# Kernel tuning notes

Hardware: AMD Instinct MI355X
Metric: run time of the kernel (lower is better)

Reference implementation:

```python
import jax, jax.numpy as jnp
import numpy as np

TOP_K = 2
CAPACITY_FACTOR = 1.0


def setup_inputs() -> dict:
    key = jax.random.key(0)
    ks = jax.random.split(key, 8)
    B, T, D, E = 4, 4096, 1024, 8
    H = 4 * D
    rn = lambda k, shape, sc: jax.random.normal(k, shape, jnp.float32) * sc
    return dict(
        x=rn(ks[0], (B, T, D), 1.0),
        noise_raw=rn(ks[1], (B, T, E), 1.0),  # replaces torch.randn_like
        Wr=rn(ks[2], (D, E), D ** -0.5), br=jnp.zeros((E,), jnp.float32),
        Wn=rn(ks[3], (D, E), D ** -0.5), bn=jnp.zeros((E,), jnp.float32),
        W1=rn(ks[4], (E, D, H), D ** -0.5), b1=jnp.zeros((E, H), jnp.float32),
        W2=rn(ks[5], (E, H, D), H ** -0.5), b2=jnp.zeros((E, D), jnp.float32),
    )


def reference(x, noise_raw, Wr, br, Wn, bn, W1, b1, W2, b2):
    B, T, D = x.shape
    E = Wr.shape[1]
    N = B * T

    # --- NoisyTopkRouter ---
    logits = x @ Wr + br                               # [B,T,E]
    noise_logits = x @ Wn + bn                         # [B,T,E]
    noisy = logits + noise_raw * jax.nn.softplus(noise_logits)
    top_vals, top_idx = jax.lax.top_k(noisy, TOP_K)    # [B,T,K]
    # softmax over (-inf)-masked sparse logits == softmax over the top-k values
    probs_k = jax.nn.softmax(top_vals, axis=-1)        # [B,T,K]
    onehot = jax.nn.one_hot(top_idx, E, dtype=x.dtype) # [B,T,K,E]
    router = jnp.einsum('btk,btke->bte', probs_k, onehot)  # sparse router probs

    # --- dispatch with capacity limit (first-come in flat token order) ---
    flat_x = x.reshape(N, D)
    flat_router = router.reshape(N, E)
    mask = onehot.reshape(N, TOP_K, E).sum(1) > 0      # [N,E] token n routed to expert e
    capacity = int(N * TOP_K / E * CAPACITY_FACTOR)
    # stable argsort brings selected tokens (key 0) first, preserving flat order
    order = jnp.argsort(jnp.where(mask, 0, 1), axis=0)             # [N,E]
    limited = order[:capacity].T                                   # [E,C] token ids (padded with unselected)
    keep = jnp.take_along_axis(mask, order[:capacity], axis=0).T   # [E,C] valid slots

    # --- grouped expert FFN ---
    xg = flat_x[limited]                                            # [E,C,D]
    h = jax.nn.relu(jnp.einsum('ecd,edh->ech', xg, W1) + b1[:, None, :])
    out_e = jnp.einsum('ech,ehd->ecd', h, W2) + b2[:, None, :]      # [E,C,D]
    # dropout is identity in eval mode

    # --- combine (scatter-add with gating; padded slots gated to 0) ---
    gate = flat_router[limited, jnp.arange(E)[:, None]] * keep.astype(x.dtype)  # [E,C]
    updates = jnp.zeros_like(flat_x).at[limited.reshape(-1)].add(
        (out_e * gate[..., None]).reshape(-1, D))
    return updates.reshape(B, T, D)
```

## Files before the change

### kernel.cpp

```cpp
#include <hip/hip_runtime.h>
#include <hip/hip_bf16.h>

namespace {
constexpr int kD = 1024, kE = 8, kH = 4096;
constexpr int kN = 16384;
constexpr int kCap = 4096;
}

typedef __attribute__((ext_vector_type(8))) short short8;
typedef __attribute__((ext_vector_type(4))) float f32x4;

static __device__ __forceinline__ unsigned short f2bf(float f) {
    __hip_bfloat16 h = __float2bfloat16(f);
    unsigned short s;
    __builtin_memcpy(&s, &h, 2);
    return s;
}

static __device__ __forceinline__ void gload_lds16(const unsigned short* g, unsigned short* l) {
    __builtin_amdgcn_global_load_lds(
        (const __attribute__((address_space(1))) unsigned int*)g,
        (__attribute__((address_space(3))) unsigned int*)l, 16, 0, 0);
}

__global__ __launch_bounds__(256) void moe_tcvt2(
    const float* __restrict__ W1, unsigned short* __restrict__ W1t,
    const float* __restrict__ W2, unsigned short* __restrict__ W2t)
{
    const int z = blockIdx.z;
    const float* src;
    unsigned short* dst;
    int R, C, bx, by;
    if (z < kE) {
        src = W1 + (size_t)z * kD * kH; dst = W1t + (size_t)z * kD * kH;
        R = kD; C = kH; bx = blockIdx.x % (kH / 64); by = blockIdx.x / (kH / 64);
    } else {
        src = W2 + (size_t)(z - kE) * kH * kD; dst = W2t + (size_t)(z - kE) * kH * kD;
        R = kH; C = kD; bx = blockIdx.x % (kD / 64); by = blockIdx.x / (kD / 64);
    }
    const int c0 = bx * 64, r0 = by * 64;
    __shared__ float t[64][68];
    const int tid = (int)threadIdx.x;
    const int tr = tid >> 2;
    const int tc = (tid & 3) * 16;
    #pragma unroll
    for (int j = 0; j < 4; ++j) {
        const float4 v = *(const float4*)(src + (size_t)(r0 + tr) * C + c0 + tc + j * 4);
        *(float4*)&t[tr][tc + j * 4] = v;
    }
    __syncthreads();
    unsigned short o[16];
    #pragma unroll
    for (int j = 0; j < 16; ++j) o[j] = f2bf(t[tc + j][tr]);
    unsigned short* dp = dst + (size_t)(c0 + tr) * R + r0 + tc;
    *(short8*)dp = *(const short8*)&o[0];
    *(short8*)(dp + 8) = *(const short8*)&o[8];
}

__global__ __launch_bounds__(256) void moe_router(
    const float* __restrict__ x, const float* __restrict__ noise_raw,
    const float* __restrict__ Wr, const float* __restrict__ br,
    const float* __restrict__ Wn, const float* __restrict__ bn,
    int2* __restrict__ topIdx, float2* __restrict__ topProb,
    unsigned short* __restrict__ xb, float* __restrict__ out)
{
    const int wave = threadIdx.x >> 6;
    const int lane = threadIdx.x & 63;
    const int n = blockIdx.x * 4 + wave;
    const float* xr = x + (size_t)n * kD;
    unsigned short* xbr = xb + (size_t)n * kD;
    float* outr = out + (size_t)n * kD;

    float accr[kE], accn[kE];
    #pragma unroll
    for (int e = 0; e < kE; ++e) { accr[e] = 0.f; accn[e] = 0.f; }

    const float4 z4 = make_float4(0.f, 0.f, 0.f, 0.f);
    #pragma unroll
    for (int c = 0; c < 4; ++c) {
        const int d0 = c * 256 + lane * 4;
        const float4 xv = *(const float4*)(xr + d0);
        *(float4*)(outr + d0) = z4;
        short4 bv;
        bv.x = (short)f2bf(xv.x); bv.y = (short)f2bf(xv.y);
        bv.z = (short)f2bf(xv.z); bv.w = (short)f2bf(xv.w);
        *(short4*)(xbr + d0) = bv;
        const float xs[4] = {xv.x, xv.y, xv.z, xv.w};
        #pragma unroll
        for (int j = 0; j < 4; ++j) {
            const float4* wr4 = (const float4*)(Wr + (size_t)(d0 + j) * kE);
            const float4* wn4 = (const float4*)(Wn + (size_t)(d0 + j) * kE);
            const float4 r0 = wr4[0], r1 = wr4[1];
            const float4 m0 = wn4[0], m1 = wn4[1];
            const float xj = xs[j];
            accr[0] += xj * r0.x; accr[1] += xj * r0.y; accr[2] += xj * r0.z; accr[3] += xj * r0.w;
            accr[4] += xj * r1.x; accr[5] += xj * r1.y; accr[6] += xj * r1.z; accr[7] += xj * r1.w;
            accn[0] += xj * m0.x; accn[1] += xj * m0.y; accn[2] += xj * m0.z; accn[3] += xj * m0.w;
            accn[4] += xj * m1.x; accn[5] += xj * m1.y; accn[6] += xj * m1.z; accn[7] += xj * m1.w;
        }
    }
    #pragma unroll
    for (int e = 0; e < kE; ++e) {
        #pragma unroll
        for (int off = 32; off >= 1; off >>= 1) {
            accr[e] += __shfl_xor(accr[e], off, 64);
            accn[e] += __shfl_xor(accn[e], off, 64);
        }
    }
    if (lane == 0) {
        float noisy[kE];
        #pragma unroll
        for (int e = 0; e < kE; ++e) {
            const float lg = accr[e] + br[e];
            const float nl = accn[e] + bn[e];
            const float sp = fmaxf(nl, 0.f) + log1pf(expf(-fabsf(nl)));
            noisy[e] = lg + noise_raw[(size_t)n * kE + e] * sp;
        }
        int i0 = 0;
        #pragma unroll
        for (int e = 1; e < kE; ++e) if (noisy[e] > noisy[i0]) i0 = e;
        int i1 = (i0 == 0) ? 1 : 0;
        #pragma unroll
        for (int e = 0; e < kE; ++e) if (e != i0 && noisy[e] > noisy[i1]) i1 = e;
        const float ex = expf(noisy[i1] - noisy[i0]);
        topIdx[n] = make_int2(i0, i1);
        topProb[n] = make_float2(1.f / (1.f + ex), ex / (1.f + ex));
    }
}

__global__ __launch_bounds__(256) void moe_dispatch(
    const int2* __restrict__ topIdx, const float2* __restrict__ topProb,
    int* __restrict__ tokList, float* __restrict__ gateList, int* __restrict__ cnt)
{
    const int e = blockIdx.x;
    const int lane = threadIdx.x & 63;
    const int wq = threadIdx.x >> 6;
    const int tpw = kN / 4;
    const unsigned long long below = (lane == 0) ? 0ull : ((~0ull) >> (64 - lane));
    __shared__ int cw[4];

    int mycnt = 0;
    for (int it = 0; it < tpw / 64; ++it) {
        const int n = wq * tpw + it * 64 + lane;
        const int2 ti = topIdx[n];
        const bool sel = (ti.x == e) || (ti.y == e);
        mycnt += __popcll(__ballot(sel));
    }
    if (lane == 0) cw[wq] = mycnt;
    __syncthreads();
    int base = 0;
    #pragma unroll
    for (int q = 0; q < 4; ++q) if (q < wq) base += cw[q];

    for (int it = 0; it < tpw / 64; ++it) {
        const int n = wq * tpw + it * 64 + lane;
        const int2 ti = topIdx[n];
        const float2 tp = topProb[n];
        const bool sel = (ti.x == e) || (ti.y == e);
        const float g = (ti.x == e) ? tp.x : tp.y;
        const unsigned long long m = __ballot(sel);
        if (sel) {
            const int slot = base + __popcll(m & below);
            if (slot < kCap) { tokList[e * kCap + slot] = n; gateList[e * kCap + slot] = g; }
        }
        base += __popcll(m);
    }
    if (threadIdx.x == 0) {
        int tot = cw[0] + cw[1] + cw[2] + cw[3];
        cnt[e] = tot < kCap ? tot : kCap;
    }
}

static __device__ __forceinline__ void remap_mn(int gx, int& mblk, int& nblk)
{
    const int l = blockIdx.y * gx + blockIdx.x;
    const int xcd = l & 7;
    const int pos = l >> 3;
    nblk = pos % gx;
    mblk = xcd + 8 * (pos / gx);
}

#define WAITV(N) asm volatile("s_waitcnt vmcnt(" #N ")" ::: "memory")
#define BARRIER_FENCE() do { __builtin_amdgcn_s_barrier(); asm volatile("" ::: "memory"); } while (0)

#define RD_A(DST, MS)                                                        \
    _Pragma("unroll")                                                        \
    for (int m_ = 0; m_ < 4; ++m_) {                                         \
        const int r_ = (wrow + ((MS) * 4 + m_) * 16 + l15) * 64;             \
        DST[m_][0] = *(const short8*)&As[buf][r_ + cbu0];                    \
        DST[m_][1] = *(const short8*)&As[buf][r_ + cbu1];                    \
    }
#define RD_B(DST, NS)                                                        \
    _Pragma("unroll")                                                        \
    for (int n_ = 0; n_ < 2; ++n_) {                                         \
        const int r_ = (wcol + ((NS) * 2 + n_) * 16 + l15) * 64;             \
        DST[n_][0] = *(const short8*)&Bs[buf][r_ + cbu0];                    \
        DST[n_][1] = *(const short8*)&Bs[buf][r_ + cbu1];                    \
    }
#define QMFMA(AF, BF, MS, NS)                                                \
    do {                                                                     \
        __builtin_amdgcn_s_setprio(1);                                       \
        _Pragma("unroll")                                                    \
        for (int kk_ = 0; kk_ < 2; ++kk_)                                    \
            _Pragma("unroll")                                                \
            for (int m_ = 0; m_ < 4; ++m_)                                   \
                _Pragma("unroll")                                            \
                for (int n_ = 0; n_ < 2; ++n_)                               \
                    acc[(MS) * 4 + m_][(NS) * 2 + n_] =                      \
                        __builtin_amdgcn_mfma_f32_16x16x32_bf16(             \
                            AF[m_][kk_], BF[n_][kk_],                        \
                            acc[(MS) * 4 + m_][(NS) * 2 + n_], 0, 0, 0);     \
        __builtin_amdgcn_s_setprio(0);                                       \
    } while (0)

#define KTILE_BODY()                                                               \
    do {                                                                           \
        const int buf = t & 1, nb = buf ^ 1, t1 = t + 1;                           \
        const bool iss = (t1 < nt);                                                \
        short8 a0[4][2], a1[4][2], b0[2][2], b1[2][2];                             \
                                        \
        RD_A(a0, 0); RD_B(b0, 0);                                                  \
        if (iss) { stA(0, nb, t1); stB(0, nb, t1); }                               \
        if (iss) { WAITV(6); } else { WAITV(2); }                                  \
        BARRIER_FENCE();                                                           \
        QMFMA(a0, b0, 0, 0);                                                       \
                                         \
        RD_A(a1, 1);                                                               \
        if (iss) stA(1, nb, t1);                                                   \
        if (iss) { WAITV(6); } else { WAITV(0); }                                  \
        BARRIER_FENCE();                                                           \
        QMFMA(a1, b0, 1, 0);                                                       \
               \
        RD_B(b1, 1);                                                               \
        if (iss) stB(1, nb, t1);                                                   \
        if (iss) { WAITV(4); } else { WAITV(0); }                                  \
        BARRIER_FENCE();                                                           \
        QMFMA(a1, b1, 1, 1);                                                       \
        QMFMA(a0, b1, 0, 1);                                                       \
    } while (0)

__global__ __launch_bounds__(512, 2) void moe_ffn1_g(
    const unsigned short* __restrict__ xb, const unsigned short* __restrict__ W1t,
    const float* __restrict__ b1,
    const int* __restrict__ tokList, const int* __restrict__ cnt,
    unsigned short* __restrict__ Hbuf, int e_base)
{
    const int e = e_base + blockIdx.z;
    const int count = cnt[e];
    int mblk, nblk;
    remap_mn((int)gridDim.x, mblk, nblk);
    const int m0 = mblk * 256;
    if (m0 >= count) return;
    const int n0 = nblk * 256;

    __shared__ unsigned short shmem[4 * 256 * 64];
    auto As = reinterpret_cast<unsigned short (*)[256 * 64]>(shmem);
    auto Bs = reinterpret_cast<unsigned short (*)[256 * 64]>(shmem + 2 * 256 * 64);

    const int tid = (int)threadIdx.x, lane = tid & 63, w = tid >> 6;
    const int wm = w >> 2, wg = w & 3, wn = w & 3;
    const int wrow = wm * 128, wcol = wn * 64;
    const int l15 = lane & 15, g = lane >> 4;
    const int rswz = l15 & 7;
    const int cbu0 = ((0 + g) ^ rswz) * 8;
    const int cbu1 = ((4 + g) ^ rswz) * 8;

    const int* tok = tokList + e * kCap;
    const unsigned short* We = W1t + (size_t)e * kD * kH;

    const unsigned short* aS[2][2];
    const unsigned short* bS[2][2];
    unsigned aD[2][2], bD[2][2];
    #pragma unroll
    for (int ms = 0; ms < 2; ++ms)
        #pragma unroll
        for (int ld = 0; ld < 2; ++ld) {
            const int flat = (wg * 2 + ld) * 64 + lane;
            const int rl = wm * 128 + ms * 64 + (flat >> 3);
            const int c = (flat & 7) ^ (rl & 7);
            int am = m0 + rl; if (am >= count) am = count - 1;
            aS[ms][ld] = xb + (size_t)tok[am] * kD + c * 8;
            aD[ms][ld] = (wm * 128 + ms * 64) * 64 + (wg * 2 + ld) * 512;
        }
    #pragma unroll
    for (int ns = 0; ns < 2; ++ns)
        #pragma unroll
        for (int ld = 0; ld < 2; ++ld) {
            const int flat = (wm * 2 + ld) * 64 + lane;
            const int rl = wn * 64 + ns * 32 + (flat >> 3);
            const int c = (flat & 7) ^ (rl & 7);
            bS[ns][ld] = We + (size_t)(n0 + rl) * kD + c * 8;
            bD[ns][ld] = (wn * 64 + ns * 32) * 64 + (wm * 2 + ld) * 512;
        }

    f32x4 acc[8][4] = {};

    auto stA = [&](int ms, int nb, int t1) {
        gload_lds16(aS[ms][0] + t1 * 64, &As[nb][aD[ms][0]]);
        gload_lds16(aS[ms][1] + t1 * 64, &As[nb][aD[ms][1]]);
    };
    auto stB = [&](int ns, int nb, int t1) {
        gload_lds16(bS[ns][0] + t1 * 64, &Bs[nb][bD[ns][0]]);
        gload_lds16(bS[ns][1] + t1 * 64, &Bs[nb][bD[ns][1]]);
    };

    constexpr int nt = kD / 64;
    stA(0, 0, 0); stB(0, 0, 0); stA(1, 0, 0); stB(1, 0, 0);
    WAITV(4);
    BARRIER_FENCE();

    for (int t = 0; t < nt; ++t) {
        KTILE_BODY();
    }

    const float* be = b1 + (size_t)e * kH + n0;
    unsigned short* H = Hbuf + (size_t)blockIdx.z * kCap * kH;
    unsigned short* tile = shmem;
    __syncthreads();
    #pragma unroll
    for (int p = 0; p < 2; ++p) {
        if (wm == p) {
            #pragma unroll
            for (int mm = 0; mm < 8; ++mm)
                #pragma unroll
                for (int i = 0; i < 4; ++i) {
                    const int rl = mm * 16 + g * 4 + i;
                    #pragma unroll
                    for (int nn = 0; nn < 4; ++nn) {
                        const int c = wcol + nn * 16 + l15;
                        tile[rl * 264 + c] = f2bf(fmaxf(acc[mm][nn][i] + be[c], 0.f));
                    }
                }
        }
        __syncthreads();
        #pragma unroll
        for (int j = 0; j < 8; ++j) {
            const int rl = j * 16 + w * 2 + (lane >> 5);
            const int r = m0 + p * 128 + rl;
            const int ch = lane & 31;
            if (r < count) {
                const short8 v = *(const short8*)&tile[rl * 264 + ch * 8];
                *(short8*)(H + (size_t)r * kH + n0 + ch * 8) = v;
            }
        }
        __syncthreads();
    }
}

__global__ __launch_bounds__(512, 2) void moe_ffn2_g(
    const unsigned short* __restrict__ Hbuf, const unsigned short* __restrict__ W2t,
    const float* __restrict__ b2,
    const int* __restrict__ tokList, const float* __restrict__ gateList,
    const int* __restrict__ cnt, float* __restrict__ out, int e_base)
{
    const int e = e_base + blockIdx.z;
    const int count = cnt[e];
    int mblk, nblk;
    remap_mn((int)gridDim.x, mblk, nblk);
    const int m0 = mblk * 256;
    if (m0 >= count) return;
    const int n0 = nblk * 256;

    __shared__ unsigned short As[2][256 * 64];
    __shared__ unsigned short Bs[2][256 * 64];

    const int tid = (int)threadIdx.x, lane = tid & 63, w = tid >> 6;
    const int wm = w >> 2, wg = w & 3, wn = w & 3;
    const int wrow = wm * 128, wcol = wn * 64;
    const int l15 = lane & 15, g = lane >> 4;
    const int rswz = l15 & 7;
    const int cbu0 = ((0 + g) ^ rswz) * 8;
    const int cbu1 = ((4 + g) ^ rswz) * 8;

    const unsigned short* H = Hbuf + (size_t)blockIdx.z * kCap * kH;
    const unsigned short* We = W2t + (size_t)e * kH * kD;

    const unsigned short* aS[2][2];
    const unsigned short* bS[2][2];
    unsigned aD[2][2], bD[2][2];
    #pragma unroll
    for (int ms = 0; ms < 2; ++ms)
        #pragma unroll
        for (int ld = 0; ld < 2; ++ld) {
            const int flat = (wg * 2 + ld) * 64 + lane;
            const int rl = wm * 128 + ms * 64 + (flat >> 3);
            const int c = (flat & 7) ^ (rl & 7);
            aS[ms][ld] = H + (size_t)(m0 + rl) * kH + c * 8;
            aD[ms][ld] = (wm * 128 + ms * 64) * 64 + (wg * 2 + ld) * 512;
        }
    #pragma unroll
    for (int ns = 0; ns < 2; ++ns)
        #pragma unroll
        for (int ld = 0; ld < 2; ++ld) {
            const int flat = (wm * 2 + ld) * 64 + lane;
            const int rl = wn * 64 + ns * 32 + (flat >> 3);
            const int c = (flat & 7) ^ (rl & 7);
            bS[ns][ld] = We + (size_t)(n0 + rl) * kH + c * 8;
            bD[ns][ld] = (wn * 64 + ns * 32) * 64 + (wm * 2 + ld) * 512;
        }

    f32x4 acc[8][4] = {};

    auto stA = [&](int ms, int nb, int t1) {
        gload_lds16(aS[ms][0] + t1 * 64, &As[nb][aD[ms][0]]);
        gload_lds16(aS[ms][1] + t1 * 64, &As[nb][aD[ms][1]]);
    };
    auto stB = [&](int ns, int nb, int t1) {
        gload_lds16(bS[ns][0] + t1 * 64, &Bs[nb][bD[ns][0]]);
        gload_lds16(bS[ns][1] + t1 * 64, &Bs[nb][bD[ns][1]]);
    };

    constexpr int nt = kH / 64;
    stA(0, 0, 0); stB(0, 0, 0); stA(1, 0, 0); stB(1, 0, 0);
    WAITV(4);
    BARRIER_FENCE();

    for (int t = 0; t < nt; ++t) {
        KTILE_BODY();
    }

    const float* be = b2 + (size_t)e * kD + n0;
    const int* tok = tokList + e * kCap;
    const float* gate = gateList + e * kCap;
    #pragma unroll
    for (int mm = 0; mm < 8; ++mm) {
        #pragma unroll
        for (int i = 0; i < 4; ++i) {
            const int r = m0 + wrow + mm * 16 + g * 4 + i;
            if (r >= count) continue;
            const int tokn = tok[r];
            const float gr = gate[r];
            float* orow = out + (size_t)tokn * kD + n0;
            #pragma unroll
            for (int nn = 0; nn < 4; ++nn) {
                const int c = wcol + nn * 16 + l15;
                atomicAdd(orow + c, (acc[mm][nn][i] + be[c]) * gr);
            }
        }
    }
}

extern "C" void kernel_launch(void* const* d_in, const int* in_sizes, int n_in,
                              void* d_out, int out_size, void* d_ws, size_t ws_size,
                              hipStream_t stream)
{
    const float* x         = (const float*)d_in[0];
    const float* noise_raw = (const float*)d_in[1];
    const float* Wr        = (const float*)d_in[2];
    const float* br        = (const float*)d_in[3];
    const float* Wn        = (const float*)d_in[4];
    const float* bn        = (const float*)d_in[5];
    const float* W1        = (const float*)d_in[6];
    const float* b1        = (const float*)d_in[7];
    const float* W2        = (const float*)d_in[8];
    const float* b2        = (const float*)d_in[9];
    float* out = (float*)d_out;

    char* ws = (char*)d_ws;
    size_t off = 0;
    auto alloc = [&](size_t bytes) -> void* {
        void* p = ws + off;
        off = (off + bytes + 255) & ~(size_t)255;
        return p;
    };
    int2*   topIdx   = (int2*)  alloc((size_t)kN * sizeof(int2));
    float2* topProb  = (float2*)alloc((size_t)kN * sizeof(float2));
    int*    tokList  = (int*)   alloc((size_t)kE * kCap * sizeof(int));
    float*  gateList = (float*) alloc((size_t)kE * kCap * sizeof(float));
    int*    cnt      = (int*)   alloc((size_t)kE * sizeof(int));

    unsigned short* xb  = (unsigned short*)alloc((size_t)kN * kD * 2);
    unsigned short* W1t = (unsigned short*)alloc((size_t)kE * kD * kH * 2);
    unsigned short* W2t = (unsigned short*)alloc((size_t)kE * kH * kD * 2);

    const size_t HB = (size_t)kCap * kH * 2;
    size_t rem = (ws_size > off) ? ws_size - off : 0;
    int G = (int)(rem / HB);
    if (G > kE) G = kE;
    if (G < 1) G = 1;
    unsigned short* Hbuf = (unsigned short*)(ws + off);

    moe_router<<<kN / 4, 256, 0, stream>>>(x, noise_raw, Wr, br, Wn, bn, topIdx, topProb, xb, out);
    moe_dispatch<<<kE, 256, 0, stream>>>(topIdx, topProb, tokList, gateList, cnt);
    moe_tcvt2<<<dim3(1024, 1, 2 * kE), 256, 0, stream>>>(W1, W1t, W2, W2t);

    for (int e0 = 0; e0 < kE; e0 += G) {
        const int gz = (kE - e0 < G) ? (kE - e0) : G;
        moe_ffn1_g<<<dim3(kH / 256, kCap / 256, gz), 512, 0, stream>>>(
            xb, W1t, b1, tokList, cnt, Hbuf, e0);
        moe_ffn2_g<<<dim3(kD / 256, kCap / 256, gz), 512, 0, stream>>>(
            Hbuf, W2t, b2, tokList, gateList, cnt, out, e0);
    }
}
```

Baseline: 955.2 us.

## Load A operand directly from global into registers, keep only B in LDS

Both expert GEMM kernels now load A-fragments (gathered token rows or hidden rows) straight from global memory into registers, one k-tile ahead, instead of staging them through LDS. Only the weight (B) tile is still double-buffered in LDS, which halves LDS traffic and capacity and drops two barriers per k-tile. The trade-off is that A rows are re-read by the four wave columns without LDS sharing, adding global/L2 traffic and register pressure, and the global load latency must be hidden by a single tile of MFMA work.

After: 1.577 ms. 1.65x slower.

```diff
diff --git a/kernel.cpp b/kernel.cpp
--- a/kernel.cpp
+++ b/kernel.cpp
@@ -183,20 +183,19 @@
 #define WAITV(N) asm volatile("s_waitcnt vmcnt(" #N ")" ::: "memory")
 #define BARRIER_FENCE() do { __builtin_amdgcn_s_barrier(); asm volatile("" ::: "memory"); } while (0)
 
-#define RD_A(DST, MS)                                                        \
-    _Pragma("unroll")                                                        \
-    for (int m_ = 0; m_ < 4; ++m_) {                                         \
-        const int r_ = (wrow + ((MS) * 4 + m_) * 16 + l15) * 64;             \
-        DST[m_][0] = *(const short8*)&As[buf][r_ + cbu0];                    \
-        DST[m_][1] = *(const short8*)&As[buf][r_ + cbu1];                    \
-    }
-#define RD_B(DST, NS)                                                        \
+#define RD_Bf(DST, NS)                                                       \
     _Pragma("unroll")                                                        \
     for (int n_ = 0; n_ < 2; ++n_) {                                         \
         const int r_ = (wcol + ((NS) * 2 + n_) * 16 + l15) * 64;             \
         DST[n_][0] = *(const short8*)&Bs[buf][r_ + cbu0];                    \
         DST[n_][1] = *(const short8*)&Bs[buf][r_ + cbu1];                    \
     }
+#define LD_A(DST, MS, KOFF)                                                  \
+    _Pragma("unroll")                                                        \
+    for (int m_ = 0; m_ < 4; ++m_)                                           \
+        _Pragma("unroll")                                                    \
+        for (int kk_ = 0; kk_ < 2; ++kk_)                                    \
+            DST[m_][kk_] = *(const short8*)(aRow[(MS) * 4 + m_] + (KOFF) + kk_ * 32 + g * 8);
 #define QMFMA(AF, BF, MS, NS)                                                \
     do {                                                                     \
         __builtin_amdgcn_s_setprio(1);                                       \
@@ -213,30 +212,20 @@
         __builtin_amdgcn_s_setprio(0);                                       \
     } while (0)
 
-#define KTILE_BODY()                                                               \
+#define KTILE_ADIRECT()                                                            \
     do {                                                                           \
         const int buf = t & 1, nb = buf ^ 1, t1 = t + 1;                           \
         const bool iss = (t1 < nt);                                                \
-        short8 a0[4][2], a1[4][2], b0[2][2], b1[2][2];                             \
-                                        \
-        RD_A(a0, 0); RD_B(b0, 0);                                                  \
-        if (iss) { stA(0, nb, t1); stB(0, nb, t1); }                               \
-        if (iss) { WAITV(6); } else { WAITV(2); }                                  \
+        RD_Bf(fb0, 0); RD_Bf(fb1, 1);                  \
+        if (iss) { stB(0, nb, t1); stB(1, nb, t1); }        \
+        QMFMA(fa0, fb0, 0, 0);                                                     \
+        QMFMA(fa0, fb1, 0, 1);                                                     \
+        LD_A(fa1, 1, t * 64);                                                      \
+        QMFMA(fa1, fb0, 1, 0);                                                     \
+        QMFMA(fa1, fb1, 1, 1);                                                     \
+        asm volatile("" ::: "memory");                   \
+        if (iss) { LD_A(fa0, 0, t1 * 64); WAITV(8); } else { WAITV(0); }           \
         BARRIER_FENCE();                                                           \
-        QMFMA(a0, b0, 0, 0);                                                       \
-                                         \
-        RD_A(a1, 1);                                                               \
-        if (iss) stA(1, nb, t1);                                                   \
-        if (iss) { WAITV(6); } else { WAITV(0); }                                  \
-        BARRIER_FENCE();                                                           \
-        QMFMA(a1, b0, 1, 0);                                                       \
-               \
-        RD_B(b1, 1);                                                               \
-        if (iss) stB(1, nb, t1);                                                   \
-        if (iss) { WAITV(4); } else { WAITV(0); }                                  \
-        BARRIER_FENCE();                                                           \
-        QMFMA(a1, b1, 1, 1);                                                       \
-        QMFMA(a0, b1, 0, 1);                                                       \
     } while (0)
 
 __global__ __launch_bounds__(512, 2) void moe_ffn1_g(
@@ -253,12 +242,11 @@
     if (m0 >= count) return;
     const int n0 = nblk * 256;
 
-    __shared__ unsigned short shmem[4 * 256 * 64];
-    auto As = reinterpret_cast<unsigned short (*)[256 * 64]>(shmem);
-    auto Bs = reinterpret_cast<unsigned short (*)[256 * 64]>(shmem + 2 * 256 * 64);
+    __shared__ unsigned short shmem[128 * 264];
+    auto Bs = reinterpret_cast<unsigned short (*)[256 * 64]>(shmem);
 
     const int tid = (int)threadIdx.x, lane = tid & 63, w = tid >> 6;
-    const int wm = w >> 2, wg = w & 3, wn = w & 3;
+    const int wm = w >> 2, wn = w & 3;
     const int wrow = wm * 128, wcol = wn * 64;
     const int l15 = lane & 15, g = lane >> 4;
     const int rswz = l15 & 7;
@@ -268,20 +256,16 @@
     const int* tok = tokList + e * kCap;
     const unsigned short* We = W1t + (size_t)e * kD * kH;
 
-    const unsigned short* aS[2][2];
+    const unsigned short* aRow[8];
+    #pragma unroll
+    for (int j = 0; j < 8; ++j) {
+        int r = m0 + wrow + j * 16 + l15;
+        if (r >= count) r = count - 1;
+        aRow[j] = xb + (size_t)tok[r] * kD;
+    }
+
     const unsigned short* bS[2][2];
-    unsigned aD[2][2], bD[2][2];
-    #pragma unroll
-    for (int ms = 0; ms < 2; ++ms)
-        #pragma unroll
-        for (int ld = 0; ld < 2; ++ld) {
-            const int flat = (wg * 2 + ld) * 64 + lane;
-            const int rl = wm * 128 + ms * 64 + (flat >> 3);
-            const int c = (flat & 7) ^ (rl & 7);
-            int am = m0 + rl; if (am >= count) am = count - 1;
-            aS[ms][ld] = xb + (size_t)tok[am] * kD + c * 8;
-            aD[ms][ld] = (wm * 128 + ms * 64) * 64 + (wg * 2 + ld) * 512;
-        }
+    unsigned bD[2][2];
     #pragma unroll
     for (int ns = 0; ns < 2; ++ns)
         #pragma unroll
@@ -294,23 +278,21 @@
         }
 
     f32x4 acc[8][4] = {};
-
-    auto stA = [&](int ms, int nb, int t1) {
-        gload_lds16(aS[ms][0] + t1 * 64, &As[nb][aD[ms][0]]);
-        gload_lds16(aS[ms][1] + t1 * 64, &As[nb][aD[ms][1]]);
-    };
+    short8 fa0[4][2], fa1[4][2], fb0[2][2], fb1[2][2];
+
     auto stB = [&](int ns, int nb, int t1) {
         gload_lds16(bS[ns][0] + t1 * 64, &Bs[nb][bD[ns][0]]);
         gload_lds16(bS[ns][1] + t1 * 64, &Bs[nb][bD[ns][1]]);
     };
 
     constexpr int nt = kD / 64;
-    stA(0, 0, 0); stB(0, 0, 0); stA(1, 0, 0); stB(1, 0, 0);
-    WAITV(4);
+    stB(0, 0, 0); stB(1, 0, 0);
+    WAITV(0);
     BARRIER_FENCE();
+    LD_A(fa0, 0, 0);
 
     for (int t = 0; t < nt; ++t) {
-        KTILE_BODY();
+        KTILE_ADIRECT();
     }
 
     const float* be = b1 + (size_t)e * kH + n0;
@@ -361,11 +343,11 @@
     if (m0 >= count) return;
     const int n0 = nblk * 256;
 
-    __shared__ unsigned short As[2][256 * 64];
-    __shared__ unsigned short Bs[2][256 * 64];
+    __shared__ unsigned short shmem[2 * 256 * 64];
+    auto Bs = reinterpret_cast<unsigned short (*)[256 * 64]>(shmem);
 
     const int tid = (int)threadIdx.x, lane = tid & 63, w = tid >> 6;
-    const int wm = w >> 2, wg = w & 3, wn = w & 3;
+    const int wm = w >> 2, wn = w & 3;
     const int wrow = wm * 128, wcol = wn * 64;
     const int l15 = lane & 15, g = lane >> 4;
     const int rswz = l15 & 7;
@@ -375,19 +357,16 @@
     const unsigned short* H = Hbuf + (size_t)blockIdx.z * kCap * kH;
     const unsigned short* We = W2t + (size_t)e * kH * kD;
 
-    const unsigned short* aS[2][2];
+    const unsigned short* aRow[8];
+    #pragma unroll
+    for (int j = 0; j < 8; ++j) {
+        int r = m0 + wrow + j * 16 + l15;
+        if (r >= count) r = count - 1;
+        aRow[j] = H + (size_t)r * kH;
+    }
+
     const unsigned short* bS[2][2];
-    unsigned aD[2][2], bD[2][2];
-    #pragma unroll
-    for (int ms = 0; ms < 2; ++ms)
-        #pragma unroll
-        for (int ld = 0; ld < 2; ++ld) {
-            const int flat = (wg * 2 + ld) * 64 + lane;
-            const int rl = wm * 128 + ms * 64 + (flat >> 3);
-            const int c = (flat & 7) ^ (rl & 7);
-            aS[ms][ld] = H + (size_t)(m0 + rl) * kH + c * 8;
-            aD[ms][ld] = (wm * 128 + ms * 64) * 64 + (wg * 2 + ld) * 512;
-        }
+    unsigned bD[2][2];
     #pragma unroll
     for (int ns = 0; ns < 2; ++ns)
         #pragma unroll
@@ -400,23 +379,21 @@
         }
 
     f32x4 acc[8][4] = {};
-
-    auto stA = [&](int ms, int nb, int t1) {
-        gload_lds16(aS[ms][0] + t1 * 64, &As[nb][aD[ms][0]]);
-        gload_lds16(aS[ms][1] + t1 * 64, &As[nb][aD[ms][1]]);
-    };
+    short8 fa0[4][2], fa1[4][2], fb0[2][2], fb1[2][2];
+
     auto stB = [&](int ns, int nb, int t1) {
         gload_lds16(bS[ns][0] + t1 * 64, &Bs[nb][bD[ns][0]]);
         gload_lds16(bS[ns][1] + t1 * 64, &Bs[nb][bD[ns][1]]);
     };
 
     constexpr int nt = kH / 64;
-    stA(0, 0, 0); stB(0, 0, 0); stA(1, 0, 0); stB(1, 0, 0);
-    WAITV(4);
+    stB(0, 0, 0); stB(1, 0, 0);
+    WAITV(0);
     BARRIER_FENCE();
+    LD_A(fa0, 0, 0);
 
     for (int t = 0; t < nt; ++t) {
-        KTILE_BODY();
+        KTILE_ADIRECT();
     }
 
     const float* be = b2 + (size_t)e * kD + n0;
```
